# Kernel tuning notes

Measured on AMD Instinct MI355X. Metric: run time of the kernel, lower is better.

## Reference

```python
import jax, jax.numpy as jnp
import numpy as np

NUM_SEQ, B, T, F, S, OUT = 4, 256, 64, 32, 512, 1


def setup_inputs() -> dict:
    key = jax.random.key(0)
    k = jax.random.split(key, 6)
    return {
        "inputs": jax.random.normal(k[0], (NUM_SEQ, B, T, F), dtype=jnp.float32),
        "W_cell": jax.random.normal(k[1], (NUM_SEQ, F + S, S), dtype=jnp.float32) * 0.05,
        "b_cell": jnp.zeros((NUM_SEQ, S), dtype=jnp.float32),
        "W_comb": jax.random.normal(k[2], (NUM_SEQ - 1, 2 * S, 1), dtype=jnp.float32) * 0.05,
        "b_comb": jnp.zeros((NUM_SEQ - 1, 1), dtype=jnp.float32),
        "W_out": jax.random.normal(k[3], (S, OUT), dtype=jnp.float32) * 0.05,
    }


def reference(inputs, W_cell, b_cell, W_comb, b_comb, W_out):
    # inputs: [num_seq, B, T, F]. Lanes are processed sequentially; lane i>0
    # gates its running state against lane i-1's stored per-step states.
    num_seq, bsz = inputs.shape[0], inputs.shape[1]
    state_size = W_cell.shape[-1]
    prev_states = None  # [T, B, S] states of previous lane
    final_states = []
    for i in range(num_seq):
        xs = jnp.swapaxes(inputs[i], 0, 1)  # [T, B, F]
        Wc, bc = W_cell[i], b_cell[i]
        h0 = jnp.zeros((bsz, state_size), dtype=inputs.dtype)
        if i == 0:
            def step(h, xt, Wc=Wc, bc=bc):
                h_new = jnp.tanh(jnp.concatenate([xt, h], axis=-1) @ Wc + bc)
                return h_new, h_new
            _, states = jax.lax.scan(step, h0, xs)
        else:
            Wg, bg = W_comb[i - 1], b_comb[i - 1]
            def step(h, x, Wc=Wc, bc=bc, Wg=Wg, bg=bg):
                xt, ph = x
                w = jax.nn.sigmoid(jnp.concatenate([h, ph], axis=-1) @ Wg + bg)  # [B,1]
                hc = w * h + (1.0 - w) * ph
                h_new = jnp.tanh(jnp.concatenate([xt, hc], axis=-1) @ Wc + bc)
                return h_new, h_new
            _, states = jax.lax.scan(step, h0, (xs, prev_states))
        prev_states = states  # [T, B, S]
        final_states.append(states[-1])
    final = jnp.concatenate(final_states, axis=0)  # [num_seq*B, S]
    out = final @ W_out  # no bias, matching tf.layers.dense(use_bias=False)
    return out.reshape(-1, num_seq, W_out.shape[1])  # [B, num_seq, OUT]
```

## Files before the change

### kernel.cpp

```cpp
#include <hip/hip_runtime.h>
#include <math.h>

#define NSEQ 4
#define BATCH 256
#define T 64
#define FIN 32
#define S 512
#define KTOT 544

#define NT 512
#define NWG 256
#define RPG 16
#define SW 128
#define DEPTH 4
#define NKT 17

#define RING_SZ  (4ull * DEPTH * BATCH * S)
#define OUTP_OFF RING_SZ
#define CTL_OFF  (RING_SZ + 16384ull)

#define FLAG_MAGIC 0x13572468u

#define AS 552

typedef __attribute__((ext_vector_type(8))) short short8;
typedef __attribute__((ext_vector_type(4))) float f32x4;
typedef __attribute__((ext_vector_type(4))) unsigned u32x4;

__device__ __forceinline__ unsigned short bf_hi(float f) {
  return (unsigned short)(__float_as_uint(f) >> 16);
}
__device__ __forceinline__ float bf_hi_f(float f) {
  return __uint_as_float(__float_as_uint(f) & 0xFFFF0000u);
}
__device__ __forceinline__ unsigned umin4(u32x4 v) {
  unsigned a = v[0] < v[1] ? v[0] : v[1];
  unsigned b = v[2] < v[3] ? v[2] : v[3];
  return a < b ? a : b;
}

__device__ __forceinline__ void cstoreu_glb(unsigned* p, unsigned v) {
  asm volatile("global_store_dword %0, %1, off sc0 sc1" :: "v"(p), "v"(v) : "memory");
}
__device__ __forceinline__ void cstore4_glb(unsigned* p, u32x4 v) {
  asm volatile("global_store_dwordx4 %0, %1, off sc0 sc1" :: "v"(p), "v"(v) : "memory");
}
__device__ __forceinline__ unsigned cldu_glb(const unsigned* p) {
  unsigned v;
  asm volatile("global_load_dword %0, %1, off sc0 sc1\n\ts_waitcnt vmcnt(0)"
               : "=v"(v) : "v"(p) : "memory");
  return v;
}
__device__ __forceinline__ u32x4 cld4_glb(const unsigned* p) {
  u32x4 v;
  asm volatile("global_load_dwordx4 %0, %1, off sc0 sc1\n\ts_waitcnt vmcnt(0)"
               : "=v"(v) : "v"(p) : "memory");
  return v;
}
__device__ __forceinline__ void cld3x4_glb(u32x4* a, u32x4* b, u32x4* c,
                                           const unsigned* pa, const unsigned* pb,
                                           const unsigned* pc) {
  asm volatile(
      "global_load_dwordx4 %0, %3, off sc0 sc1\n\t"
      "global_load_dwordx4 %1, %4, off sc0 sc1\n\t"
      "global_load_dwordx4 %2, %5, off sc0 sc1\n\t"
      "s_waitcnt vmcnt(0)"
      : "=&v"(*a), "=&v"(*b), "=&v"(*c)
      : "v"(pa), "v"(pb), "v"(pc) : "memory");
}
__device__ __forceinline__ void cstore1(float* p, float v) {
  asm volatile("global_store_dword %0, %1, off sc0 sc1" :: "v"(p), "v"(v) : "memory");
}
__device__ __forceinline__ float cload1(const float* p) {
  float v;
  asm volatile("global_load_dword %0, %1, off sc0 sc1\n\ts_waitcnt vmcnt(0)"
               : "=v"(v) : "v"(p) : "memory");
  return v;
}
__device__ __forceinline__ void cload_row(float4* d, const float* p) {
  asm volatile(
      "global_load_dwordx4 %0, %4, off sc0 sc1\n\t"
      "global_load_dwordx4 %1, %4, off offset:512 sc0 sc1\n\t"
      "global_load_dwordx4 %2, %4, off offset:1024 sc0 sc1\n\t"
      "global_load_dwordx4 %3, %4, off offset:1536 sc0 sc1\n\t"
      "s_waitcnt vmcnt(0)"
      : "=&v"(d[0]), "=&v"(d[1]), "=&v"(d[2]), "=&v"(d[3])
      : "v"(p) : "memory");
}
__device__ __forceinline__ void cload_row2(float4* h, float4* q,
                                           const float* ph, const float* pp) {
  asm volatile(
      "global_load_dwordx4 %0, %8, off sc0 sc1\n\t"
      "global_load_dwordx4 %1, %8, off offset:512 sc0 sc1\n\t"
      "global_load_dwordx4 %2, %8, off offset:1024 sc0 sc1\n\t"
      "global_load_dwordx4 %3, %8, off offset:1536 sc0 sc1\n\t"
      "global_load_dwordx4 %4, %9, off sc0 sc1\n\t"
      "global_load_dwordx4 %5, %9, off offset:512 sc0 sc1\n\t"
      "global_load_dwordx4 %6, %9, off offset:1024 sc0 sc1\n\t"
      "global_load_dwordx4 %7, %9, off offset:1536 sc0 sc1\n\t"
      "s_waitcnt vmcnt(0)"
      : "=&v"(h[0]), "=&v"(h[1]), "=&v"(h[2]), "=&v"(h[3]),
        "=&v"(q[0]), "=&v"(q[1]), "=&v"(q[2]), "=&v"(q[3])
      : "v"(ph), "v"(pp) : "memory");
}


extern "C" __global__ void __launch_bounds__(NT, 1)
rnn_mfma(const float* __restrict__ x,
         const float* __restrict__ Wcell,
         const float* __restrict__ bcell,
         const float* __restrict__ Wcomb,
         const float* __restrict__ bcomb,
         const float* __restrict__ Wout,
         float* __restrict__ out,
         float* __restrict__ ws)
{
  const int b    = blockIdx.x;
  const int o    = b >> 3;
  const int grp  = (b & 7) + 8 * (o >> 4);
  const int sub  = o & 15;
  const int lane = sub >> 2;
  const int sl   = sub & 3;
  const int gid  = lane * 16 + grp;
  const int r0 = grp * RPG, sb = sl * SW;
  const int tid = threadIdx.x;

  __shared__ __align__(16) unsigned short A1[RPG * AS];
  __shared__ __align__(16) unsigned short A2[RPG * AS];
  __shared__ float wg_lds[2 * S];
  __shared__ float obuf[128];
  __shared__ float fbuf[64];

  float* ring = ws;
  unsigned* ctl     = (unsigned*)(ws + CTL_OFF);
  unsigned* st_own  = ctl + gid * 64;
  unsigned* st_prod = ctl + (gid - 16) * 64;
  unsigned* st_cons = ctl + (gid + 16) * 64;
  unsigned* st_mine = st_own + sl;
  const unsigned* pp_poll = (lane > 0) ? st_prod : st_own;
  const unsigned* pc_poll = (lane < 3) ? st_cons : st_own;

  if (sl == 0 && tid == 0) {
    const u32x4 z = {0u, 0u, 0u, 0u};
    cstore4_glb(st_own, z);
    asm volatile("s_waitcnt vmcnt(0)" ::: "memory");
    cstoreu_glb(st_own + 32, FLAG_MAGIC);
  }
  if (tid == 0) {
    #pragma unroll
    for (int l = 0; l < 4; ++l) {
      const unsigned* f = ctl + (l * 16 + grp) * 64 + 32;
      while (cldu_glb(f) != FLAG_MAGIC) __builtin_amdgcn_s_sleep(1);
    }
  }

  const float* Wc = Wcell + (size_t)lane * KTOT * S;
  const int wl = tid & 63, wt = tid >> 6;
  const int bn = wl & 15, q = wl >> 4;
  const int ncol = sb + wt * 16 + bn;
  short8 B1[NKT], B2[NKT];
  #pragma unroll
  for (int kt = 0; kt < NKT; ++kt) {
    short8 b1, b2;
    #pragma unroll
    for (int j = 0; j < 8; ++j) {
      const float w = Wc[(size_t)(kt * 32 + q * 8 + j) * S + ncol];
      b1[j] = (short)bf_hi(w);
      b2[j] = (short)bf_hi(w - bf_hi_f(w));
    }
    B1[kt] = b1; B2[kt] = b2;
  }
  const float bcv = bcell[lane * S + ncol];
  const float wov = Wout[ncol];
  for (int idx = tid; idx < 2 * S; idx += NT)
    wg_lds[idx] = (lane > 0) ? Wcomb[(size_t)(lane - 1) * 2 * S + idx] : 0.0f;
  const float bg = (lane > 0) ? bcomb[lane - 1] : 0.0f;
  const int grow = tid >> 5, gch = tid & 31;
  __syncthreads();

  float oacc[4] = {0.f, 0.f, 0.f, 0.f};

  for (int t = 0; t < T; ++t) {
    {
      const float f0 = x[(((size_t)lane * BATCH + r0 + grow) * T + t) * FIN + gch];
      A1[grow * AS + gch] = bf_hi(f0);
      A2[grow * AS + gch] = bf_hi(f0 - bf_hi_f(f0));
    }
    for (;;) {
      u32x4 so, sp, sc;
      cld3x4_glb(&so, &sp, &sc, st_own, pp_poll, pc_poll);
      bool ok = true;
      if (t > 0)                  ok &= (umin4(so) >= (unsigned)t);
      if (lane > 0)               ok &= (umin4(sp) >= (unsigned)(t + 1));
      if (lane < 3 && t >= DEPTH) ok &= (umin4(sc) >= (unsigned)(t - 3));
      if (ok) break;
      __builtin_amdgcn_s_sleep(1);
    }

    {
      const int row = grow;
      float4 hv[4], pv[4];
      const float* hb = ring + ((size_t)(lane * DEPTH + ((t - 1) & 3)) * BATCH + r0 + row) * S + gch * 4;
      const float* pb = ring + ((size_t)((lane - 1) * DEPTH + (t & 3)) * BATCH + r0 + row) * S + gch * 4;
      if (t > 0) {
        if (lane > 0) cload_row2(hv, pv, hb, pb);
        else          cload_row(hv, hb);
      } else {
        #pragma unroll
        for (int j = 0; j < 4; ++j) hv[j] = make_float4(0.f, 0.f, 0.f, 0.f);
        if (lane > 0) cload_row(pv, pb);
      }
      if (lane > 0) {
        float gs = 0.0f;
        #pragma unroll
        for (int j = 0; j < 4; ++j) {
          const float* wh = &wg_lds[j * 128 + gch * 4];
          const float* wp = wh + S;
          gs += hv[j].x * wh[0] + hv[j].y * wh[1] + hv[j].z * wh[2] + hv[j].w * wh[3];
          gs += pv[j].x * wp[0] + pv[j].y * wp[1] + pv[j].z * wp[2] + pv[j].w * wp[3];
        }
        gs += __shfl_xor(gs, 1);  gs += __shfl_xor(gs, 2);  gs += __shfl_xor(gs, 4);
        gs += __shfl_xor(gs, 8);  gs += __shfl_xor(gs, 16);
        const float w = 1.0f / (1.0f + __expf(-(gs + bg)));
        #pragma unroll
        for (int j = 0; j < 4; ++j) {
          hv[j].x = fmaf(w, hv[j].x - pv[j].x, pv[j].x);
          hv[j].y = fmaf(w, hv[j].y - pv[j].y, pv[j].y);
          hv[j].z = fmaf(w, hv[j].z - pv[j].z, pv[j].z);
          hv[j].w = fmaf(w, hv[j].w - pv[j].w, pv[j].w);
        }
      }
      #pragma unroll
      for (int j = 0; j < 4; ++j) {
        ushort4 h4, l4;
        h4.x = bf_hi(hv[j].x); l4.x = bf_hi(hv[j].x - bf_hi_f(hv[j].x));
        h4.y = bf_hi(hv[j].y); l4.y = bf_hi(hv[j].y - bf_hi_f(hv[j].y));
        h4.z = bf_hi(hv[j].z); l4.z = bf_hi(hv[j].z - bf_hi_f(hv[j].z));
        h4.w = bf_hi(hv[j].w); l4.w = bf_hi(hv[j].w - bf_hi_f(hv[j].w));
        const int ai = row * AS + 32 + j * 128 + gch * 4;
        *(ushort4*)&A1[ai] = h4;
        *(ushort4*)&A2[ai] = l4;
      }
    }
    __syncthreads();

    f32x4 acc = {0.f, 0.f, 0.f, 0.f};
    {
      const unsigned short* ar1 = &A1[bn * AS + q * 8];
      const unsigned short* ar2 = &A2[bn * AS + q * 8];
      #pragma unroll
      for (int kt = 0; kt < NKT; ++kt) {
        const short8 a1 = *(const short8*)(ar1 + kt * 32);
        const short8 a2 = *(const short8*)(ar2 + kt * 32);
        acc = __builtin_amdgcn_mfma_f32_16x16x32_bf16(a1, B1[kt], acc, 0, 0, 0);
        acc = __builtin_amdgcn_mfma_f32_16x16x32_bf16(a1, B2[kt], acc, 0, 0, 0);
        acc = __builtin_amdgcn_mfma_f32_16x16x32_bf16(a2, B1[kt], acc, 0, 0, 0);
      }
    }

    float* slot = ring + ((size_t)(lane * DEPTH + (t & 3)) * BATCH + r0) * S + sb;
    #pragma unroll
    for (int reg = 0; reg < 4; ++reg) {
      const float s2 = acc[reg] + bcv;
      const float aa = fabsf(s2), ee = __expf(2.0f * aa);
      const float tv = copysignf(1.0f - 2.0f / (ee + 1.0f), s2);
      cstore1(slot + (size_t)(q * 4 + reg) * S + wt * 16 + bn, tv);
      if (t == T - 1) oacc[reg] = tv * wov;
    }
    asm volatile("s_waitcnt vmcnt(0)" ::: "memory");
    __syncthreads();
    if (tid == 0) cstoreu_glb(st_mine, (unsigned)(t + 1));
  }

  #pragma unroll
  for (int reg = 0; reg < 4; ++reg) {
    float v = oacc[reg];
    v += __shfl_xor(v, 1); v += __shfl_xor(v, 2);
    v += __shfl_xor(v, 4); v += __shfl_xor(v, 8);
    if (bn == 0) obuf[wt * 16 + q * 4 + reg] = v;
  }
  __syncthreads();
  if (tid < 16) {
    float v = 0.0f;
    #pragma unroll
    for (int w = 0; w < 8; ++w) v += obuf[w * 16 + tid];
    cstore1(ws + OUTP_OFF + (size_t)((gid * 4 + sl) * 16 + tid), v);
  }
  asm volatile("s_waitcnt vmcnt(0)" ::: "memory");
  __syncthreads();
  if (tid == 0) cstoreu_glb(st_mine, (unsigned)(T + 1));
  if (sl == 0) {
    if (tid == 0)
      while (umin4(cld4_glb(st_own)) < (unsigned)(T + 1)) __builtin_amdgcn_s_sleep(1);
    __syncthreads();
    if (tid < 64) {
      const int sli = tid >> 4, r = tid & 15;
      fbuf[tid] = cload1(ws + OUTP_OFF + (size_t)((gid * 4 + sli) * 16 + r));
    }
    __syncthreads();
    if (tid < 16) {
      float s2 = 0.f;
      #pragma unroll
      for (int sli = 0; sli < 4; ++sli) s2 += fbuf[sli * 16 + tid];
      out[lane * BATCH + r0 + tid] = s2;
    }
  }
}

extern "C" void kernel_launch(void* const* d_in, const int* in_sizes, int n_in,
                              void* d_out, int out_size, void* d_ws, size_t ws_size,
                              hipStream_t stream) {
  (void)in_sizes; (void)n_in; (void)out_size; (void)ws_size;
  rnn_mfma<<<dim3(NWG), dim3(NT), 0, stream>>>(
      (const float*)d_in[0],
      (const float*)d_in[1],
      (const float*)d_in[2],
      (const float*)d_in[3],
      (const float*)d_in[4],
      (const float*)d_in[5],
      (float*)d_out,
      (float*)d_ws);
}
```

Before: 367.9 us.

## Embed step tags in ring data to replace producer flag polling

Each ring entry now stores a packed bf16 hi/lo pair whose two lowest bits hold a step tag. Consumers spin on the data itself until the tags match, instead of first polling the producer step counters, so a full flag round-trip is removed from the critical path. The ring is zeroed at start and the init handshake now checks neighbour flags. The tag bits slightly lower the precision of the low bf16 half, and the own/consumer counter poll is kept only for ring reuse from t>=4.

```diff
diff --git a/kernel.cpp b/kernel.cpp
--- a/kernel.cpp
+++ b/kernel.cpp
@@ -27,29 +27,32 @@
 typedef __attribute__((ext_vector_type(4))) float f32x4;
 typedef __attribute__((ext_vector_type(4))) unsigned u32x4;
 
-__device__ __forceinline__ unsigned short bf_hi(float f) {
-  return (unsigned short)(__float_as_uint(f) >> 16);
+__device__ __forceinline__ unsigned bf_hi(float f) {
+  return (__float_as_uint(f) >> 16);
 }
 __device__ __forceinline__ float bf_hi_f(float f) {
   return __uint_as_float(__float_as_uint(f) & 0xFFFF0000u);
+}
+__device__ __forceinline__ float rec_f(unsigned w) {
+  return __uint_as_float(w & 0xFFFF0000u) + __uint_as_float(w << 16);
 }
 __device__ __forceinline__ unsigned umin4(u32x4 v) {
   unsigned a = v[0] < v[1] ? v[0] : v[1];
   unsigned b = v[2] < v[3] ? v[2] : v[3];
   return a < b ? a : b;
 }
+__device__ __forceinline__ bool alleq4(u32x4 v, unsigned m) {
+  return v[0] == m && v[1] == m && v[2] == m && v[3] == m;
+}
+__device__ __forceinline__ unsigned step_tag(int t) {
+  return (unsigned)(((t >> 2) % 3) + 1);
+}
 
 __device__ __forceinline__ void cstoreu_glb(unsigned* p, unsigned v) {
   asm volatile("global_store_dword %0, %1, off sc0 sc1" :: "v"(p), "v"(v) : "memory");
 }
 __device__ __forceinline__ void cstore4_glb(unsigned* p, u32x4 v) {
   asm volatile("global_store_dwordx4 %0, %1, off sc0 sc1" :: "v"(p), "v"(v) : "memory");
-}
-__device__ __forceinline__ unsigned cldu_glb(const unsigned* p) {
-  unsigned v;
-  asm volatile("global_load_dword %0, %1, off sc0 sc1\n\ts_waitcnt vmcnt(0)"
-               : "=v"(v) : "v"(p) : "memory");
-  return v;
 }
 __device__ __forceinline__ u32x4 cld4_glb(const unsigned* p) {
   u32x4 v;
@@ -57,16 +60,13 @@
                : "=v"(v) : "v"(p) : "memory");
   return v;
 }
-__device__ __forceinline__ void cld3x4_glb(u32x4* a, u32x4* b, u32x4* c,
-                                           const unsigned* pa, const unsigned* pb,
-                                           const unsigned* pc) {
+__device__ __forceinline__ void cld2x4_glb(u32x4* a, u32x4* b,
+                                           const unsigned* pa, const unsigned* pb) {
   asm volatile(
-      "global_load_dwordx4 %0, %3, off sc0 sc1\n\t"
-      "global_load_dwordx4 %1, %4, off sc0 sc1\n\t"
-      "global_load_dwordx4 %2, %5, off sc0 sc1\n\t"
+      "global_load_dwordx4 %0, %2, off sc0 sc1\n\t"
+      "global_load_dwordx4 %1, %3, off sc0 sc1\n\t"
       "s_waitcnt vmcnt(0)"
-      : "=&v"(*a), "=&v"(*b), "=&v"(*c)
-      : "v"(pa), "v"(pb), "v"(pc) : "memory");
+      : "=&v"(*a), "=&v"(*b) : "v"(pa), "v"(pb) : "memory");
 }
 __device__ __forceinline__ void cstore1(float* p, float v) {
   asm volatile("global_store_dword %0, %1, off sc0 sc1" :: "v"(p), "v"(v) : "memory");
@@ -77,7 +77,7 @@
                : "=v"(v) : "v"(p) : "memory");
   return v;
 }
-__device__ __forceinline__ void cload_row(float4* d, const float* p) {
+__device__ __forceinline__ void cload_rowu(u32x4* d, const unsigned* p) {
   asm volatile(
       "global_load_dwordx4 %0, %4, off sc0 sc1\n\t"
       "global_load_dwordx4 %1, %4, off offset:512 sc0 sc1\n\t"
@@ -87,8 +87,8 @@
       : "=&v"(d[0]), "=&v"(d[1]), "=&v"(d[2]), "=&v"(d[3])
       : "v"(p) : "memory");
 }
-__device__ __forceinline__ void cload_row2(float4* h, float4* q,
-                                           const float* ph, const float* pp) {
+__device__ __forceinline__ void cload_row2u(u32x4* h, u32x4* q,
+                                            const unsigned* ph, const unsigned* pp) {
   asm volatile(
       "global_load_dwordx4 %0, %8, off sc0 sc1\n\t"
       "global_load_dwordx4 %1, %8, off offset:512 sc0 sc1\n\t"
@@ -131,26 +131,37 @@
   __shared__ float obuf[128];
   __shared__ float fbuf[64];
 
-  float* ring = ws;
+  unsigned* uring   = (unsigned*)ws;
   unsigned* ctl     = (unsigned*)(ws + CTL_OFF);
   unsigned* st_own  = ctl + gid * 64;
   unsigned* st_prod = ctl + (gid - 16) * 64;
   unsigned* st_cons = ctl + (gid + 16) * 64;
   unsigned* st_mine = st_own + sl;
-  const unsigned* pp_poll = (lane > 0) ? st_prod : st_own;
+  unsigned* flg_own  = st_own + 32;
+  unsigned* flg_prod = st_prod + 32;
+  unsigned* flg_cons = st_cons + 32;
   const unsigned* pc_poll = (lane < 3) ? st_cons : st_own;
 
-  if (sl == 0 && tid == 0) {
+  {
     const u32x4 z = {0u, 0u, 0u, 0u};
-    cstore4_glb(st_own, z);
-    asm volatile("s_waitcnt vmcnt(0)" ::: "memory");
-    cstoreu_glb(st_own + 32, FLAG_MAGIC);
-  }
+    const int zr = tid >> 5, zc4 = (tid & 31) * 4;
+    #pragma unroll
+    for (int d = 0; d < DEPTH; ++d) {
+      unsigned* p = uring + ((size_t)(lane * DEPTH + d) * BATCH + r0 + zr) * S + sb + zc4;
+      cstore4_glb(p, z);
+    }
+    if (sl == 0 && tid == 0) cstore4_glb(st_own, z);
+  }
+  asm volatile("s_waitcnt vmcnt(0)" ::: "memory");
+  __syncthreads();
   if (tid == 0) {
-    #pragma unroll
-    for (int l = 0; l < 4; ++l) {
-      const unsigned* f = ctl + (l * 16 + grp) * 64 + 32;
-      while (cldu_glb(f) != FLAG_MAGIC) __builtin_amdgcn_s_sleep(1);
+    cstoreu_glb(flg_own + sl, FLAG_MAGIC);
+    for (;;) {
+      bool ok = alleq4(cld4_glb(flg_own), FLAG_MAGIC);
+      if (lane > 0) ok &= alleq4(cld4_glb(flg_prod), FLAG_MAGIC);
+      if (lane < 3) ok &= alleq4(cld4_glb(flg_cons), FLAG_MAGIC);
+      if (ok) break;
+      __builtin_amdgcn_s_sleep(2);
     }
   }
 
@@ -183,63 +194,112 @@
   for (int t = 0; t < T; ++t) {
     {
       const float f0 = x[(((size_t)lane * BATCH + r0 + grow) * T + t) * FIN + gch];
-      A1[grow * AS + gch] = bf_hi(f0);
-      A2[grow * AS + gch] = bf_hi(f0 - bf_hi_f(f0));
-    }
-    for (;;) {
-      u32x4 so, sp, sc;
-      cld3x4_glb(&so, &sp, &sc, st_own, pp_poll, pc_poll);
-      bool ok = true;
-      if (t > 0)                  ok &= (umin4(so) >= (unsigned)t);
-      if (lane > 0)               ok &= (umin4(sp) >= (unsigned)(t + 1));
-      if (lane < 3 && t >= DEPTH) ok &= (umin4(sc) >= (unsigned)(t - 3));
-      if (ok) break;
-      __builtin_amdgcn_s_sleep(1);
+      A1[grow * AS + gch] = (unsigned short)bf_hi(f0);
+      A2[grow * AS + gch] = (unsigned short)bf_hi(f0 - bf_hi_f(f0));
+    }
+    if (t >= 4) {
+      for (;;) {
+        u32x4 so, sc;
+        cld2x4_glb(&so, &sc, st_own, pc_poll);
+        bool ok = (umin4(so) >= (unsigned)(t - 2));
+        if (lane < 3) ok &= (umin4(sc) >= (unsigned)(t - 3));
+        if (ok) break;
+        __builtin_amdgcn_s_sleep(1);
+      }
     }
 
     {
       const int row = grow;
-      float4 hv[4], pv[4];
-      const float* hb = ring + ((size_t)(lane * DEPTH + ((t - 1) & 3)) * BATCH + r0 + row) * S + gch * 4;
-      const float* pb = ring + ((size_t)((lane - 1) * DEPTH + (t & 3)) * BATCH + r0 + row) * S + gch * 4;
+      const unsigned* hb = uring + ((size_t)(lane * DEPTH + ((t - 1) & 3)) * BATCH + r0 + row) * S + gch * 4;
+      const unsigned* pb = uring + ((size_t)((lane - 1) * DEPTH + (t & 3)) * BATCH + r0 + row) * S + gch * 4;
+      const unsigned tag_h = step_tag(t - 1);
+      const unsigned tag_p = step_tag(t);
+      u32x4 hw[4], pw[4];
       if (t > 0) {
-        if (lane > 0) cload_row2(hv, pv, hb, pb);
-        else          cload_row(hv, hb);
+        if (lane > 0) {
+          for (;;) {
+            cload_row2u(hw, pw, hb, pb);
+            unsigned bad = 0u;
+            #pragma unroll
+            for (int j = 0; j < 4; ++j)
+              #pragma unroll
+              for (int e = 0; e < 4; ++e)
+                bad |= ((hw[j][e] & 3u) ^ tag_h) | ((pw[j][e] & 3u) ^ tag_p);
+            if (!bad) break;
+            __builtin_amdgcn_s_sleep(1);
+          }
+        } else {
+          for (;;) {
+            cload_rowu(hw, hb);
+            unsigned bad = 0u;
+            #pragma unroll
+            for (int j = 0; j < 4; ++j)
+              #pragma unroll
+              for (int e = 0; e < 4; ++e)
+                bad |= ((hw[j][e] & 3u) ^ tag_h);
+            if (!bad) break;
+            __builtin_amdgcn_s_sleep(1);
+          }
+        }
       } else {
         #pragma unroll
-        for (int j = 0; j < 4; ++j) hv[j] = make_float4(0.f, 0.f, 0.f, 0.f);
-        if (lane > 0) cload_row(pv, pb);
+        for (int j = 0; j < 4; ++j) hw[j] = (u32x4){0u, 0u, 0u, 0u};
+        if (lane > 0) {
+          for (;;) {
+            cload_rowu(pw, pb);
+            unsigned bad = 0u;
+            #pragma unroll
+            for (int j = 0; j < 4; ++j)
+              #pragma unroll
+              for (int e = 0; e < 4; ++e)
+                bad |= ((pw[j][e] & 3u) ^ tag_p);
+            if (!bad) break;
+            __builtin_amdgcn_s_sleep(1);
+          }
+        }
       }
+
       if (lane > 0) {
         float gs = 0.0f;
         #pragma unroll
         for (int j = 0; j < 4; ++j) {
           const float* wh = &wg_lds[j * 128 + gch * 4];
           const float* wp = wh + S;
-          gs += hv[j].x * wh[0] + hv[j].y * wh[1] + hv[j].z * wh[2] + hv[j].w * wh[3];
-          gs += pv[j].x * wp[0] + pv[j].y * wp[1] + pv[j].z * wp[2] + pv[j].w * wp[3];
+          #pragma unroll
+          for (int e = 0; e < 4; ++e)
+            gs += rec_f(hw[j][e]) * wh[e] + rec_f(pw[j][e]) * wp[e];
         }
         gs += __shfl_xor(gs, 1);  gs += __shfl_xor(gs, 2);  gs += __shfl_xor(gs, 4);
         gs += __shfl_xor(gs, 8);  gs += __shfl_xor(gs, 16);
-        const float w = 1.0f / (1.0f + __expf(-(gs + bg)));
+        const float wgt = 1.0f / (1.0f + __expf(-(gs + bg)));
         #pragma unroll
         for (int j = 0; j < 4; ++j) {
-          hv[j].x = fmaf(w, hv[j].x - pv[j].x, pv[j].x);
-          hv[j].y = fmaf(w, hv[j].y - pv[j].y, pv[j].y);
-          hv[j].z = fmaf(w, hv[j].z - pv[j].z, pv[j].z);
-          hv[j].w = fmaf(w, hv[j].w - pv[j].w, pv[j].w);
-        }
-      }
-      #pragma unroll
-      for (int j = 0; j < 4; ++j) {
-        ushort4 h4, l4;
-        h4.x = bf_hi(hv[j].x); l4.x = bf_hi(hv[j].x - bf_hi_f(hv[j].x));
-        h4.y = bf_hi(hv[j].y); l4.y = bf_hi(hv[j].y - bf_hi_f(hv[j].y));
-        h4.z = bf_hi(hv[j].z); l4.z = bf_hi(hv[j].z - bf_hi_f(hv[j].z));
-        h4.w = bf_hi(hv[j].w); l4.w = bf_hi(hv[j].w - bf_hi_f(hv[j].w));
-        const int ai = row * AS + 32 + j * 128 + gch * 4;
-        *(ushort4*)&A1[ai] = h4;
-        *(ushort4*)&A2[ai] = l4;
+          ushort4 h4, l4;
+          #pragma unroll
+          for (int e = 0; e < 4; ++e) {
+            const float hf = rec_f(hw[j][e]);
+            const float pf = rec_f(pw[j][e]);
+            const float hc = fmaf(wgt, hf - pf, pf);
+            (&h4.x)[e] = (unsigned short)bf_hi(hc);
+            (&l4.x)[e] = (unsigned short)bf_hi(hc - bf_hi_f(hc));
+          }
+          const int ai = row * AS + 32 + j * 128 + gch * 4;
+          *(ushort4*)&A1[ai] = h4;
+          *(ushort4*)&A2[ai] = l4;
+        }
+      } else {
+        #pragma unroll
+        for (int j = 0; j < 4; ++j) {
+          ushort4 h4, l4;
+          #pragma unroll
+          for (int e = 0; e < 4; ++e) {
+            (&h4.x)[e] = (unsigned short)(hw[j][e] >> 16);
+            (&l4.x)[e] = (unsigned short)(hw[j][e] & 0xFFFFu);
+          }
+          const int ai = row * AS + 32 + j * 128 + gch * 4;
+          *(ushort4*)&A1[ai] = h4;
+          *(ushort4*)&A2[ai] = l4;
+        }
       }
     }
     __syncthreads();
@@ -258,13 +318,16 @@
       }
     }
 
-    float* slot = ring + ((size_t)(lane * DEPTH + (t & 3)) * BATCH + r0) * S + sb;
+    unsigned* uslot = uring + ((size_t)(lane * DEPTH + (t & 3)) * BATCH + r0) * S + sb;
+    const unsigned tg = step_tag(t);
     #pragma unroll
     for (int reg = 0; reg < 4; ++reg) {
       const float s2 = acc[reg] + bcv;
       const float aa = fabsf(s2), ee = __expf(2.0f * aa);
       const float tv = copysignf(1.0f - 2.0f / (ee + 1.0f), s2);
-      cstore1(slot + (size_t)(q * 4 + reg) * S + wt * 16 + bn, tv);
+      const unsigned hi = bf_hi(tv);
+      const unsigned lo = (bf_hi(tv - bf_hi_f(tv)) & 0xFFFCu) | tg;
+      cstoreu_glb(uslot + (size_t)(q * 4 + reg) * S + wt * 16 + bn, (hi << 16) | lo);
       if (t == T - 1) oacc[reg] = tv * wov;
     }
     asm volatile("s_waitcnt vmcnt(0)" ::: "memory");
```

After: 394.4 us. 1.07x slower.

## Fuse dependency polling with state loads using per-row ring-slot canaries

Applied to the files above, without the earlier changes.

Replaces the separate poll-then-load step with a combined load that fetches the state rows together with per-row canary words and status counters, retrying until every canary shows the expected timestep. Each workgroup now writes per-row canaries after storing its slice of the state, and init publishes per-slice magic flags that only neighbouring lanes check. This removes one global round trip per timestep from the critical path. The cost is extra control stores each step, and whole state rows are re-read when a spin has to retry.

```diff
diff --git a/kernel.cpp b/kernel.cpp
--- a/kernel.cpp
+++ b/kernel.cpp
@@ -38,18 +38,15 @@
   unsigned b = v[2] < v[3] ? v[2] : v[3];
   return a < b ? a : b;
 }
+__device__ __forceinline__ bool alleq4(u32x4 v, unsigned m) {
+  return v[0] == m && v[1] == m && v[2] == m && v[3] == m;
+}
 
 __device__ __forceinline__ void cstoreu_glb(unsigned* p, unsigned v) {
   asm volatile("global_store_dword %0, %1, off sc0 sc1" :: "v"(p), "v"(v) : "memory");
 }
 __device__ __forceinline__ void cstore4_glb(unsigned* p, u32x4 v) {
   asm volatile("global_store_dwordx4 %0, %1, off sc0 sc1" :: "v"(p), "v"(v) : "memory");
-}
-__device__ __forceinline__ unsigned cldu_glb(const unsigned* p) {
-  unsigned v;
-  asm volatile("global_load_dword %0, %1, off sc0 sc1\n\ts_waitcnt vmcnt(0)"
-               : "=v"(v) : "v"(p) : "memory");
-  return v;
 }
 __device__ __forceinline__ u32x4 cld4_glb(const unsigned* p) {
   u32x4 v;
@@ -57,17 +54,6 @@
                : "=v"(v) : "v"(p) : "memory");
   return v;
 }
-__device__ __forceinline__ void cld3x4_glb(u32x4* a, u32x4* b, u32x4* c,
-                                           const unsigned* pa, const unsigned* pb,
-                                           const unsigned* pc) {
-  asm volatile(
-      "global_load_dwordx4 %0, %3, off sc0 sc1\n\t"
-      "global_load_dwordx4 %1, %4, off sc0 sc1\n\t"
-      "global_load_dwordx4 %2, %5, off sc0 sc1\n\t"
-      "s_waitcnt vmcnt(0)"
-      : "=&v"(*a), "=&v"(*b), "=&v"(*c)
-      : "v"(pa), "v"(pb), "v"(pc) : "memory");
-}
 __device__ __forceinline__ void cstore1(float* p, float v) {
   asm volatile("global_store_dword %0, %1, off sc0 sc1" :: "v"(p), "v"(v) : "memory");
 }
@@ -77,31 +63,65 @@
                : "=v"(v) : "v"(p) : "memory");
   return v;
 }
-__device__ __forceinline__ void cload_row(float4* d, const float* p) {
+
+__device__ __forceinline__ void ld_full(float4* h, float4* p, u32x4* hc, u32x4* pc,
+                                        u32x4* so, u32x4* sc,
+                                        const float* ph, const float* pp,
+                                        const unsigned* phc, const unsigned* ppc,
+                                        const unsigned* pso, const unsigned* psc) {
   asm volatile(
-      "global_load_dwordx4 %0, %4, off sc0 sc1\n\t"
-      "global_load_dwordx4 %1, %4, off offset:512 sc0 sc1\n\t"
-      "global_load_dwordx4 %2, %4, off offset:1024 sc0 sc1\n\t"
-      "global_load_dwordx4 %3, %4, off offset:1536 sc0 sc1\n\t"
-      "s_waitcnt vmcnt(0)"
-      : "=&v"(d[0]), "=&v"(d[1]), "=&v"(d[2]), "=&v"(d[3])
-      : "v"(p) : "memory");
-}
-__device__ __forceinline__ void cload_row2(float4* h, float4* q,
-                                           const float* ph, const float* pp) {
-  asm volatile(
-      "global_load_dwordx4 %0, %8, off sc0 sc1\n\t"
-      "global_load_dwordx4 %1, %8, off offset:512 sc0 sc1\n\t"
-      "global_load_dwordx4 %2, %8, off offset:1024 sc0 sc1\n\t"
-      "global_load_dwordx4 %3, %8, off offset:1536 sc0 sc1\n\t"
-      "global_load_dwordx4 %4, %9, off sc0 sc1\n\t"
-      "global_load_dwordx4 %5, %9, off offset:512 sc0 sc1\n\t"
-      "global_load_dwordx4 %6, %9, off offset:1024 sc0 sc1\n\t"
-      "global_load_dwordx4 %7, %9, off offset:1536 sc0 sc1\n\t"
+      "global_load_dwordx4 %0, %12, off sc0 sc1\n\t"
+      "global_load_dwordx4 %1, %12, off offset:512 sc0 sc1\n\t"
+      "global_load_dwordx4 %2, %12, off offset:1024 sc0 sc1\n\t"
+      "global_load_dwordx4 %3, %12, off offset:1536 sc0 sc1\n\t"
+      "global_load_dwordx4 %4, %13, off sc0 sc1\n\t"
+      "global_load_dwordx4 %5, %13, off offset:512 sc0 sc1\n\t"
+      "global_load_dwordx4 %6, %13, off offset:1024 sc0 sc1\n\t"
+      "global_load_dwordx4 %7, %13, off offset:1536 sc0 sc1\n\t"
+      "global_load_dwordx4 %8, %14, off sc0 sc1\n\t"
+      "global_load_dwordx4 %9, %15, off sc0 sc1\n\t"
+      "global_load_dwordx4 %10, %16, off sc0 sc1\n\t"
+      "global_load_dwordx4 %11, %17, off sc0 sc1\n\t"
       "s_waitcnt vmcnt(0)"
       : "=&v"(h[0]), "=&v"(h[1]), "=&v"(h[2]), "=&v"(h[3]),
-        "=&v"(q[0]), "=&v"(q[1]), "=&v"(q[2]), "=&v"(q[3])
-      : "v"(ph), "v"(pp) : "memory");
+        "=&v"(p[0]), "=&v"(p[1]), "=&v"(p[2]), "=&v"(p[3]),
+        "=&v"(*hc), "=&v"(*pc), "=&v"(*so), "=&v"(*sc)
+      : "v"(ph), "v"(pp), "v"(phc), "v"(ppc), "v"(pso), "v"(psc)
+      : "memory");
+}
+__device__ __forceinline__ void ld_h(float4* h, u32x4* hc, u32x4* so, u32x4* sc,
+                                     const float* ph, const unsigned* phc,
+                                     const unsigned* pso, const unsigned* psc) {
+  asm volatile(
+      "global_load_dwordx4 %0, %7, off sc0 sc1\n\t"
+      "global_load_dwordx4 %1, %7, off offset:512 sc0 sc1\n\t"
+      "global_load_dwordx4 %2, %7, off offset:1024 sc0 sc1\n\t"
+      "global_load_dwordx4 %3, %7, off offset:1536 sc0 sc1\n\t"
+      "global_load_dwordx4 %4, %8, off sc0 sc1\n\t"
+      "global_load_dwordx4 %5, %9, off sc0 sc1\n\t"
+      "global_load_dwordx4 %6, %10, off sc0 sc1\n\t"
+      "s_waitcnt vmcnt(0)"
+      : "=&v"(h[0]), "=&v"(h[1]), "=&v"(h[2]), "=&v"(h[3]),
+        "=&v"(*hc), "=&v"(*so), "=&v"(*sc)
+      : "v"(ph), "v"(phc), "v"(pso), "v"(psc)
+      : "memory");
+}
+__device__ __forceinline__ void ld_p(float4* p, u32x4* pc, u32x4* so, u32x4* sc,
+                                     const float* pp, const unsigned* ppc,
+                                     const unsigned* pso, const unsigned* psc) {
+  asm volatile(
+      "global_load_dwordx4 %0, %7, off sc0 sc1\n\t"
+      "global_load_dwordx4 %1, %7, off offset:512 sc0 sc1\n\t"
+      "global_load_dwordx4 %2, %7, off offset:1024 sc0 sc1\n\t"
+      "global_load_dwordx4 %3, %7, off offset:1536 sc0 sc1\n\t"
+      "global_load_dwordx4 %4, %8, off sc0 sc1\n\t"
+      "global_load_dwordx4 %5, %9, off sc0 sc1\n\t"
+      "global_load_dwordx4 %6, %10, off sc0 sc1\n\t"
+      "s_waitcnt vmcnt(0)"
+      : "=&v"(p[0]), "=&v"(p[1]), "=&v"(p[2]), "=&v"(p[3]),
+        "=&v"(*pc), "=&v"(*so), "=&v"(*sc)
+      : "v"(pp), "v"(ppc), "v"(pso), "v"(psc)
+      : "memory");
 }
 
 
@@ -134,23 +154,32 @@
   float* ring = ws;
   unsigned* ctl     = (unsigned*)(ws + CTL_OFF);
   unsigned* st_own  = ctl + gid * 64;
-  unsigned* st_prod = ctl + (gid - 16) * 64;
   unsigned* st_cons = ctl + (gid + 16) * 64;
   unsigned* st_mine = st_own + sl;
-  const unsigned* pp_poll = (lane > 0) ? st_prod : st_own;
-  const unsigned* pc_poll = (lane < 3) ? st_cons : st_own;
-
+  unsigned* flg_own  = st_own + 32;
+  unsigned* flg_prod = ctl + (gid - 16) * 64 + 32;
+  unsigned* flg_cons = st_cons + 32;
+  unsigned* can = ctl + 8192;
+  const unsigned* psc = (lane < 3) ? st_cons : st_own;
+
+  if (tid < 64) {
+    const int slot = tid >> 4, row = tid & 15;
+    cstoreu_glb(can + ((((lane * 4 + slot) * 16 + grp) * 16 + row) * 4 + sl), 0u);
+  }
   if (sl == 0 && tid == 0) {
     const u32x4 z = {0u, 0u, 0u, 0u};
     cstore4_glb(st_own, z);
-    asm volatile("s_waitcnt vmcnt(0)" ::: "memory");
-    cstoreu_glb(st_own + 32, FLAG_MAGIC);
-  }
+  }
+  asm volatile("s_waitcnt vmcnt(0)" ::: "memory");
+  __syncthreads();
   if (tid == 0) {
-    #pragma unroll
-    for (int l = 0; l < 4; ++l) {
-      const unsigned* f = ctl + (l * 16 + grp) * 64 + 32;
-      while (cldu_glb(f) != FLAG_MAGIC) __builtin_amdgcn_s_sleep(1);
+    cstoreu_glb(flg_own + sl, FLAG_MAGIC);
+    for (;;) {
+      bool ok = alleq4(cld4_glb(flg_own), FLAG_MAGIC);
+      if (lane > 0) ok &= alleq4(cld4_glb(flg_prod), FLAG_MAGIC);
+      if (lane < 3) ok &= alleq4(cld4_glb(flg_cons), FLAG_MAGIC);
+      if (ok) break;
+      __builtin_amdgcn_s_sleep(2);
     }
   }
 
@@ -186,30 +215,45 @@
       A1[grow * AS + gch] = bf_hi(f0);
       A2[grow * AS + gch] = bf_hi(f0 - bf_hi_f(f0));
     }
-    for (;;) {
-      u32x4 so, sp, sc;
-      cld3x4_glb(&so, &sp, &sc, st_own, pp_poll, pc_poll);
-      bool ok = true;
-      if (t > 0)                  ok &= (umin4(so) >= (unsigned)t);
-      if (lane > 0)               ok &= (umin4(sp) >= (unsigned)(t + 1));
-      if (lane < 3 && t >= DEPTH) ok &= (umin4(sc) >= (unsigned)(t - 3));
-      if (ok) break;
-      __builtin_amdgcn_s_sleep(1);
-    }
 
     {
-      const int row = grow;
       float4 hv[4], pv[4];
-      const float* hb = ring + ((size_t)(lane * DEPTH + ((t - 1) & 3)) * BATCH + r0 + row) * S + gch * 4;
-      const float* pb = ring + ((size_t)((lane - 1) * DEPTH + (t & 3)) * BATCH + r0 + row) * S + gch * 4;
+      const float* hb = ring + ((size_t)(lane * DEPTH + ((t - 1) & 3)) * BATCH + r0 + grow) * S + gch * 4;
+      const float* pb = ring + ((size_t)((lane - 1) * DEPTH + (t & 3)) * BATCH + r0 + grow) * S + gch * 4;
+      const unsigned* hce = can + (((lane * 4 + ((t - 1) & 3)) * 16 + grp) * 16 + grow) * 4;
+      const unsigned* pce = can + ((((lane - 1) * 4 + (t & 3)) * 16 + grp) * 16 + grow) * 4;
+      const unsigned th = (unsigned)t, tp = (unsigned)(t + 1);
+      u32x4 hcan, pcan, sown, scon;
       if (t > 0) {
-        if (lane > 0) cload_row2(hv, pv, hb, pb);
-        else          cload_row(hv, hb);
+        if (lane > 0) {
+          for (;;) {
+            ld_full(hv, pv, &hcan, &pcan, &sown, &scon, hb, pb, hce, pce, st_own, psc);
+            bool ok = ((int)umin4(sown) >= t - 2) && ((int)umin4(scon) >= t - 3);
+            ok &= alleq4(hcan, th) && alleq4(pcan, tp);
+            if (ok) break;
+            __builtin_amdgcn_s_sleep(1);
+          }
+        } else {
+          for (;;) {
+            ld_h(hv, &hcan, &sown, &scon, hb, hce, st_own, psc);
+            bool ok = ((int)umin4(sown) >= t - 2) && ((int)umin4(scon) >= t - 3);
+            ok &= alleq4(hcan, th);
+            if (ok) break;
+            __builtin_amdgcn_s_sleep(1);
+          }
+        }
       } else {
         #pragma unroll
         for (int j = 0; j < 4; ++j) hv[j] = make_float4(0.f, 0.f, 0.f, 0.f);
-        if (lane > 0) cload_row(pv, pb);
+        if (lane > 0) {
+          for (;;) {
+            ld_p(pv, &pcan, &sown, &scon, pb, pce, st_own, psc);
+            if (alleq4(pcan, tp)) break;
+            __builtin_amdgcn_s_sleep(1);
+          }
+        }
       }
+
       if (lane > 0) {
         float gs = 0.0f;
         #pragma unroll
@@ -237,7 +281,7 @@
         h4.y = bf_hi(hv[j].y); l4.y = bf_hi(hv[j].y - bf_hi_f(hv[j].y));
         h4.z = bf_hi(hv[j].z); l4.z = bf_hi(hv[j].z - bf_hi_f(hv[j].z));
         h4.w = bf_hi(hv[j].w); l4.w = bf_hi(hv[j].w - bf_hi_f(hv[j].w));
-        const int ai = row * AS + 32 + j * 128 + gch * 4;
+        const int ai = grow * AS + 32 + j * 128 + gch * 4;
         *(ushort4*)&A1[ai] = h4;
         *(ushort4*)&A2[ai] = l4;
       }
@@ -269,7 +313,11 @@
     }
     asm volatile("s_waitcnt vmcnt(0)" ::: "memory");
     __syncthreads();
-    if (tid == 0) cstoreu_glb(st_mine, (unsigned)(t + 1));
+    if (tid < 16)
+      cstoreu_glb(can + ((((lane * 4 + (t & 3)) * 16 + grp) * 16 + tid) * 4 + sl),
+                  (unsigned)(t + 1));
+    else if (tid == 16)
+      cstoreu_glb(st_mine, (unsigned)(t + 1));
   }
 
   #pragma unroll
```

New measurement: 356.1 us (median of 2 runs). 3.2% less time.

## Use per-row completion flags, stage own state slice in LDS, vectorize ring stores

Applied to the files above, without the earlier changes.

Replaces the coarse per-group step counters with per-row, per-slice completion flags, so each thread row waits only for the rows it actually reads. Each workgroup's own state slice is kept in LDS and reused the next step, and the ring write becomes one coalesced dwordx4 store per thread after an LDS transpose. The MFMA chain is also split across two accumulators to shorten the dependency chain. In exchange it adds more flag stores, wider polling (four loads per poll), an extra barrier per step, and more complex startup handshaking.

```diff
diff --git a/kernel.cpp b/kernel.cpp
--- a/kernel.cpp
+++ b/kernel.cpp
@@ -38,6 +38,9 @@
   unsigned b = v[2] < v[3] ? v[2] : v[3];
   return a < b ? a : b;
 }
+__device__ __forceinline__ bool alleq4(u32x4 v, unsigned m) {
+  return v[0] == m && v[1] == m && v[2] == m && v[3] == m;
+}
 
 __device__ __forceinline__ void cstoreu_glb(unsigned* p, unsigned v) {
   asm volatile("global_store_dword %0, %1, off sc0 sc1" :: "v"(p), "v"(v) : "memory");
@@ -45,11 +48,8 @@
 __device__ __forceinline__ void cstore4_glb(unsigned* p, u32x4 v) {
   asm volatile("global_store_dwordx4 %0, %1, off sc0 sc1" :: "v"(p), "v"(v) : "memory");
 }
-__device__ __forceinline__ unsigned cldu_glb(const unsigned* p) {
-  unsigned v;
-  asm volatile("global_load_dword %0, %1, off sc0 sc1\n\ts_waitcnt vmcnt(0)"
-               : "=v"(v) : "v"(p) : "memory");
-  return v;
+__device__ __forceinline__ void cstore4f_glb(float* p, f32x4 v) {
+  asm volatile("global_store_dwordx4 %0, %1, off sc0 sc1" :: "v"(p), "v"(v) : "memory");
 }
 __device__ __forceinline__ u32x4 cld4_glb(const unsigned* p) {
   u32x4 v;
@@ -57,25 +57,52 @@
                : "=v"(v) : "v"(p) : "memory");
   return v;
 }
-__device__ __forceinline__ void cld3x4_glb(u32x4* a, u32x4* b, u32x4* c,
-                                           const unsigned* pa, const unsigned* pb,
-                                           const unsigned* pc) {
+__device__ __forceinline__ void cstore1(float* p, float v) {
+  asm volatile("global_store_dword %0, %1, off sc0 sc1" :: "v"(p), "v"(v) : "memory");
+}
+__device__ __forceinline__ float cload1(const float* p) {
+  float v;
+  asm volatile("global_load_dword %0, %1, off sc0 sc1\n\ts_waitcnt vmcnt(0)"
+               : "=v"(v) : "v"(p) : "memory");
+  return v;
+}
+__device__ __forceinline__ void poll4(u32x4* a, u32x4* b, u32x4* c, u32x4* d,
+                                      const unsigned* pa, const unsigned* pb,
+                                      const unsigned* pc, const unsigned* pd) {
+  asm volatile(
+      "global_load_dwordx4 %0, %4, off sc0 sc1\n\t"
+      "global_load_dwordx4 %1, %5, off sc0 sc1\n\t"
+      "global_load_dwordx4 %2, %6, off sc0 sc1\n\t"
+      "global_load_dwordx4 %3, %7, off sc0 sc1\n\t"
+      "s_waitcnt vmcnt(0)"
+      : "=&v"(*a), "=&v"(*b), "=&v"(*c), "=&v"(*d)
+      : "v"(pa), "v"(pb), "v"(pc), "v"(pd) : "memory");
+}
+__device__ __forceinline__ void ld_h3p4(float4* h3, float4* p,
+                                        const float* ph0, const float* ph1,
+                                        const float* ph2, const float* pp) {
+  asm volatile(
+      "global_load_dwordx4 %0, %7, off sc0 sc1\n\t"
+      "global_load_dwordx4 %1, %8, off sc0 sc1\n\t"
+      "global_load_dwordx4 %2, %9, off sc0 sc1\n\t"
+      "global_load_dwordx4 %3, %10, off sc0 sc1\n\t"
+      "global_load_dwordx4 %4, %10, off offset:512 sc0 sc1\n\t"
+      "global_load_dwordx4 %5, %10, off offset:1024 sc0 sc1\n\t"
+      "global_load_dwordx4 %6, %10, off offset:1536 sc0 sc1\n\t"
+      "s_waitcnt vmcnt(0)"
+      : "=&v"(h3[0]), "=&v"(h3[1]), "=&v"(h3[2]),
+        "=&v"(p[0]), "=&v"(p[1]), "=&v"(p[2]), "=&v"(p[3])
+      : "v"(ph0), "v"(ph1), "v"(ph2), "v"(pp) : "memory");
+}
+__device__ __forceinline__ void ld_h3(float4* h3, const float* ph0,
+                                      const float* ph1, const float* ph2) {
   asm volatile(
       "global_load_dwordx4 %0, %3, off sc0 sc1\n\t"
       "global_load_dwordx4 %1, %4, off sc0 sc1\n\t"
       "global_load_dwordx4 %2, %5, off sc0 sc1\n\t"
       "s_waitcnt vmcnt(0)"
-      : "=&v"(*a), "=&v"(*b), "=&v"(*c)
-      : "v"(pa), "v"(pb), "v"(pc) : "memory");
-}
-__device__ __forceinline__ void cstore1(float* p, float v) {
-  asm volatile("global_store_dword %0, %1, off sc0 sc1" :: "v"(p), "v"(v) : "memory");
-}
-__device__ __forceinline__ float cload1(const float* p) {
-  float v;
-  asm volatile("global_load_dword %0, %1, off sc0 sc1\n\ts_waitcnt vmcnt(0)"
-               : "=v"(v) : "v"(p) : "memory");
-  return v;
+      : "=&v"(h3[0]), "=&v"(h3[1]), "=&v"(h3[2])
+      : "v"(ph0), "v"(ph1), "v"(ph2) : "memory");
 }
 __device__ __forceinline__ void cload_row(float4* d, const float* p) {
   asm volatile(
@@ -86,22 +113,6 @@
       "s_waitcnt vmcnt(0)"
       : "=&v"(d[0]), "=&v"(d[1]), "=&v"(d[2]), "=&v"(d[3])
       : "v"(p) : "memory");
-}
-__device__ __forceinline__ void cload_row2(float4* h, float4* q,
-                                           const float* ph, const float* pp) {
-  asm volatile(
-      "global_load_dwordx4 %0, %8, off sc0 sc1\n\t"
-      "global_load_dwordx4 %1, %8, off offset:512 sc0 sc1\n\t"
-      "global_load_dwordx4 %2, %8, off offset:1024 sc0 sc1\n\t"
-      "global_load_dwordx4 %3, %8, off offset:1536 sc0 sc1\n\t"
-      "global_load_dwordx4 %4, %9, off sc0 sc1\n\t"
-      "global_load_dwordx4 %5, %9, off offset:512 sc0 sc1\n\t"
-      "global_load_dwordx4 %6, %9, off offset:1024 sc0 sc1\n\t"
-      "global_load_dwordx4 %7, %9, off offset:1536 sc0 sc1\n\t"
-      "s_waitcnt vmcnt(0)"
-      : "=&v"(h[0]), "=&v"(h[1]), "=&v"(h[2]), "=&v"(h[3]),
-        "=&v"(q[0]), "=&v"(q[1]), "=&v"(q[2]), "=&v"(q[3])
-      : "v"(ph), "v"(pp) : "memory");
 }
 
 
@@ -127,6 +138,7 @@
 
   __shared__ __align__(16) unsigned short A1[RPG * AS];
   __shared__ __align__(16) unsigned short A2[RPG * AS];
+  __shared__ __align__(16) float h_lds[RPG * SW];
   __shared__ float wg_lds[2 * S];
   __shared__ float obuf[128];
   __shared__ float fbuf[64];
@@ -134,23 +146,32 @@
   float* ring = ws;
   unsigned* ctl     = (unsigned*)(ws + CTL_OFF);
   unsigned* st_own  = ctl + gid * 64;
-  unsigned* st_prod = ctl + (gid - 16) * 64;
   unsigned* st_cons = ctl + (gid + 16) * 64;
   unsigned* st_mine = st_own + sl;
-  const unsigned* pp_poll = (lane > 0) ? st_prod : st_own;
-  const unsigned* pc_poll = (lane < 3) ? st_cons : st_own;
-
+  unsigned* flg_own  = st_own + 32;
+  unsigned* flg_prod = ctl + (gid - 16) * 64 + 32;
+  unsigned* flg_cons = st_cons + 32;
+  unsigned* can = ctl + 8192;
+  const unsigned* psc = (lane < 3) ? st_cons : st_own;
+
+  if (tid < 64) {
+    const int slot = tid >> 4, row = tid & 15;
+    cstoreu_glb(can + ((((lane * 4 + slot) * 16 + grp) * 16 + row) * 4 + sl), 0u);
+  }
   if (sl == 0 && tid == 0) {
     const u32x4 z = {0u, 0u, 0u, 0u};
     cstore4_glb(st_own, z);
-    asm volatile("s_waitcnt vmcnt(0)" ::: "memory");
-    cstoreu_glb(st_own + 32, FLAG_MAGIC);
-  }
+  }
+  asm volatile("s_waitcnt vmcnt(0)" ::: "memory");
+  __syncthreads();
   if (tid == 0) {
-    #pragma unroll
-    for (int l = 0; l < 4; ++l) {
-      const unsigned* f = ctl + (l * 16 + grp) * 64 + 32;
-      while (cldu_glb(f) != FLAG_MAGIC) __builtin_amdgcn_s_sleep(1);
+    cstoreu_glb(flg_own + sl, FLAG_MAGIC);
+    for (;;) {
+      bool ok = alleq4(cld4_glb(flg_own), FLAG_MAGIC);
+      if (lane > 0) ok &= alleq4(cld4_glb(flg_prod), FLAG_MAGIC);
+      if (lane < 3) ok &= alleq4(cld4_glb(flg_cons), FLAG_MAGIC);
+      if (ok) break;
+      __builtin_amdgcn_s_sleep(2);
     }
   }
 
@@ -186,30 +207,55 @@
       A1[grow * AS + gch] = bf_hi(f0);
       A2[grow * AS + gch] = bf_hi(f0 - bf_hi_f(f0));
     }
-    for (;;) {
-      u32x4 so, sp, sc;
-      cld3x4_glb(&so, &sp, &sc, st_own, pp_poll, pc_poll);
-      bool ok = true;
-      if (t > 0)                  ok &= (umin4(so) >= (unsigned)t);
-      if (lane > 0)               ok &= (umin4(sp) >= (unsigned)(t + 1));
-      if (lane < 3 && t >= DEPTH) ok &= (umin4(sc) >= (unsigned)(t - 3));
-      if (ok) break;
-      __builtin_amdgcn_s_sleep(1);
-    }
 
     {
-      const int row = grow;
+      const unsigned* hce = (t > 0)
+          ? can + (((lane * 4 + ((t - 1) & 3)) * 16 + grp) * 16 + grow) * 4
+          : st_own;
+      const unsigned* pce = (lane > 0)
+          ? can + ((((lane - 1) * 4 + (t & 3)) * 16 + grp) * 16 + grow) * 4
+          : st_own;
+      for (;;) {
+        u32x4 hc, pc, so, sc;
+        poll4(&hc, &pc, &so, &sc, hce, pce, st_own, psc);
+        bool ok = ((int)umin4(so) >= t - 2);
+        if (lane < 3) ok &= ((int)umin4(sc) >= t - 3);
+        if (t > 0)    ok &= alleq4(hc, (unsigned)t);
+        if (lane > 0) ok &= alleq4(pc, (unsigned)(t + 1));
+        if (ok) break;
+        __builtin_amdgcn_s_sleep(1);
+      }
+
       float4 hv[4], pv[4];
-      const float* hb = ring + ((size_t)(lane * DEPTH + ((t - 1) & 3)) * BATCH + r0 + row) * S + gch * 4;
-      const float* pb = ring + ((size_t)((lane - 1) * DEPTH + (t & 3)) * BATCH + r0 + row) * S + gch * 4;
+      const float* hrow = ring + ((size_t)(lane * DEPTH + ((t - 1) & 3)) * BATCH + r0 + grow) * S + gch * 4;
+      const float* prow = ring + ((size_t)((lane - 1) * DEPTH + (t & 3)) * BATCH + r0 + grow) * S + gch * 4;
       if (t > 0) {
-        if (lane > 0) cload_row2(hv, pv, hb, pb);
-        else          cload_row(hv, hb);
+        const float4 ownv = *(const float4*)&h_lds[grow * SW + gch * 4];
+        float4 h3[3];
+        switch (sl) {
+          case 0:
+            if (lane > 0) ld_h3p4(h3, pv, hrow + 1*SW, hrow + 2*SW, hrow + 3*SW, prow);
+            else          ld_h3(h3, hrow + 1*SW, hrow + 2*SW, hrow + 3*SW);
+            hv[1] = h3[0]; hv[2] = h3[1]; hv[3] = h3[2]; hv[0] = ownv; break;
+          case 1:
+            if (lane > 0) ld_h3p4(h3, pv, hrow + 0*SW, hrow + 2*SW, hrow + 3*SW, prow);
+            else          ld_h3(h3, hrow + 0*SW, hrow + 2*SW, hrow + 3*SW);
+            hv[0] = h3[0]; hv[2] = h3[1]; hv[3] = h3[2]; hv[1] = ownv; break;
+          case 2:
+            if (lane > 0) ld_h3p4(h3, pv, hrow + 0*SW, hrow + 1*SW, hrow + 3*SW, prow);
+            else          ld_h3(h3, hrow + 0*SW, hrow + 1*SW, hrow + 3*SW);
+            hv[0] = h3[0]; hv[1] = h3[1]; hv[3] = h3[2]; hv[2] = ownv; break;
+          default:
+            if (lane > 0) ld_h3p4(h3, pv, hrow + 0*SW, hrow + 1*SW, hrow + 2*SW, prow);
+            else          ld_h3(h3, hrow + 0*SW, hrow + 1*SW, hrow + 2*SW);
+            hv[0] = h3[0]; hv[1] = h3[1]; hv[2] = h3[2]; hv[3] = ownv; break;
+        }
       } else {
         #pragma unroll
         for (int j = 0; j < 4; ++j) hv[j] = make_float4(0.f, 0.f, 0.f, 0.f);
-        if (lane > 0) cload_row(pv, pb);
-      }
+        if (lane > 0) cload_row(pv, prow);
+      }
+
       if (lane > 0) {
         float gs = 0.0f;
         #pragma unroll
@@ -237,14 +283,14 @@
         h4.y = bf_hi(hv[j].y); l4.y = bf_hi(hv[j].y - bf_hi_f(hv[j].y));
         h4.z = bf_hi(hv[j].z); l4.z = bf_hi(hv[j].z - bf_hi_f(hv[j].z));
         h4.w = bf_hi(hv[j].w); l4.w = bf_hi(hv[j].w - bf_hi_f(hv[j].w));
-        const int ai = row * AS + 32 + j * 128 + gch * 4;
+        const int ai = grow * AS + 32 + j * 128 + gch * 4;
         *(ushort4*)&A1[ai] = h4;
         *(ushort4*)&A2[ai] = l4;
       }
     }
     __syncthreads();
 
-    f32x4 acc = {0.f, 0.f, 0.f, 0.f};
+    f32x4 acc0 = {0.f, 0.f, 0.f, 0.f}, acc1 = {0.f, 0.f, 0.f, 0.f};
     {
       const unsigned short* ar1 = &A1[bn * AS + q * 8];
       const unsigned short* ar2 = &A2[bn * AS + q * 8];
@@ -252,24 +298,40 @@
       for (int kt = 0; kt < NKT; ++kt) {
         const short8 a1 = *(const short8*)(ar1 + kt * 32);
         const short8 a2 = *(const short8*)(ar2 + kt * 32);
-        acc = __builtin_amdgcn_mfma_f32_16x16x32_bf16(a1, B1[kt], acc, 0, 0, 0);
-        acc = __builtin_amdgcn_mfma_f32_16x16x32_bf16(a1, B2[kt], acc, 0, 0, 0);
-        acc = __builtin_amdgcn_mfma_f32_16x16x32_bf16(a2, B1[kt], acc, 0, 0, 0);
-      }
-    }
-
-    float* slot = ring + ((size_t)(lane * DEPTH + (t & 3)) * BATCH + r0) * S + sb;
+        if (kt < 9) {
+          acc0 = __builtin_amdgcn_mfma_f32_16x16x32_bf16(a1, B1[kt], acc0, 0, 0, 0);
+          acc0 = __builtin_amdgcn_mfma_f32_16x16x32_bf16(a1, B2[kt], acc0, 0, 0, 0);
+          acc0 = __builtin_amdgcn_mfma_f32_16x16x32_bf16(a2, B1[kt], acc0, 0, 0, 0);
+        } else {
+          acc1 = __builtin_amdgcn_mfma_f32_16x16x32_bf16(a1, B1[kt], acc1, 0, 0, 0);
+          acc1 = __builtin_amdgcn_mfma_f32_16x16x32_bf16(a1, B2[kt], acc1, 0, 0, 0);
+          acc1 = __builtin_amdgcn_mfma_f32_16x16x32_bf16(a2, B1[kt], acc1, 0, 0, 0);
+        }
+      }
+    }
+
     #pragma unroll
     for (int reg = 0; reg < 4; ++reg) {
-      const float s2 = acc[reg] + bcv;
+      const float s2 = acc0[reg] + acc1[reg] + bcv;
       const float aa = fabsf(s2), ee = __expf(2.0f * aa);
       const float tv = copysignf(1.0f - 2.0f / (ee + 1.0f), s2);
-      cstore1(slot + (size_t)(q * 4 + reg) * S + wt * 16 + bn, tv);
+      h_lds[(q * 4 + reg) * SW + wt * 16 + bn] = tv;
       if (t == T - 1) oacc[reg] = tv * wov;
     }
+    __syncthreads();
+
+    {
+      const f32x4 v = *(const f32x4*)&h_lds[grow * SW + gch * 4];
+      float* dst = ring + ((size_t)(lane * DEPTH + (t & 3)) * BATCH + r0 + grow) * S + sb + gch * 4;
+      cstore4f_glb(dst, v);
+    }
     asm volatile("s_waitcnt vmcnt(0)" ::: "memory");
     __syncthreads();
-    if (tid == 0) cstoreu_glb(st_mine, (unsigned)(t + 1));
+    if (tid < 16)
+      cstoreu_glb(can + ((((lane * 4 + (t & 3)) * 16 + grp) * 16 + tid) * 4 + sl),
+                  (unsigned)(t + 1));
+    else if (tid == 16)
+      cstoreu_glb(st_mine, (unsigned)(t + 1));
   }
 
   #pragma unroll
```

Result: slower. 388.9 us (+5.7%).
